# Kernel tuning notes

Hardware: AMD Instinct MI355X
Metric: run time of the kernel (lower is better)

Reference implementation:

```python
import jax, jax.numpy as jnp
import numpy as np

B, L, C, H, W = 4, 64, 64, 32, 32


def setup_inputs() -> dict:
    key = jax.random.key(0)
    ks = jax.random.split(key, 12)
    r_min, r_max = 0.8, 0.99
    u1 = jax.random.uniform(ks[0], (C, H))
    u2 = jax.random.uniform(ks[1], (C, H))
    nu_log = jnp.log(-0.5 * jnp.log(u1 * (r_max ** 2 - r_min ** 2) + r_min ** 2))
    theta_log = jnp.log(u2 * 2.0 * np.pi)
    lam_abs = jnp.exp(-jnp.exp(nu_log))  # |lambda| = exp(-exp(nu_log))
    gamma_log = jnp.log(jnp.sqrt(1.0 - lam_abs ** 2))
    params_log = jnp.concatenate([nu_log, theta_log, gamma_log], axis=0)  # (3C, H)
    s = 1.0 / np.sqrt(C)
    Wb_r = jax.random.normal(ks[2], (C, C)) * s
    Wb_i = jax.random.normal(ks[3], (C, C)) * s
    bb_r = jax.random.normal(ks[4], (C,)) * 0.01
    bb_i = jax.random.normal(ks[5], (C,)) * 0.01
    Wc_r = jax.random.normal(ks[6], (C, C)) * s
    Wc_i = jax.random.normal(ks[7], (C, C)) * s
    bc_r = jax.random.normal(ks[8], (C,)) * 0.01
    bc_i = jax.random.normal(ks[9], (C,)) * 0.01
    ln_w = jnp.ones((H, W), jnp.float32)
    ln_b = jnp.zeros((H, W), jnp.float32)
    x = jax.random.normal(ks[10], (B, L, C, H, W), jnp.float32)
    return dict(x=x, params_log=params_log, Wb_r=Wb_r, Wb_i=Wb_i, bb_r=bb_r, bb_i=bb_i,
                Wc_r=Wc_r, Wc_i=Wc_i, bc_r=bc_r, bc_i=bc_i, ln_w=ln_w, ln_b=ln_b)


def _convlru(x, params_log, Wb_r, Wb_i, bb_r, bb_i, Wc_r, Wc_i, bc_r, bc_i, ln_w, ln_b):
    c = params_log.shape[0] // 3
    p = jnp.exp(params_log)
    nu, theta, gamma = p[:c], p[c:2 * c], p[2 * c:]          # each (C, H)
    lamb = jnp.exp(-nu + 1j * theta)                          # (C, H) complex64
    # FFT over spatial dims
    h = jnp.fft.fft2(x.astype(jnp.complex64), axes=(-2, -1))  # (B,L,C,H,W)
    # proj_B: complex 1x1x1 conv == channel mixing
    Wb = Wb_r + 1j * Wb_i
    bb = bb_r + 1j * bb_i
    h = jnp.einsum('blchw,oc->blohw', h, Wb) + bb[None, None, :, None, None]
    h = h * gamma[None, None, :, :, None].astype(h.dtype)
    # parallel linear recurrence: h[t] = lamb * h[t-1] + h[t]
    a = jnp.broadcast_to(lamb[None, None, :, :, None], h.shape)

    def op(e1, e2):
        a1, b1 = e1
        a2, b2 = e2
        return (a1 * a2, a2 * b1 + b2)

    _, h = jax.lax.associative_scan(op, (a, h), axis=1)
    last_hidden_out = h[:, -1:]
    h = jnp.fft.ifft2(h, axes=(-2, -1))
    # proj_C
    Wc = Wc_r + 1j * Wc_i
    bc = bc_r + 1j * bc_i
    h = jnp.einsum('blchw,oc->blohw', h, Wc) + bc[None, None, :, None, None]
    h = h.real
    # LayerNorm over (H, W)
    mu = h.mean(axis=(-2, -1), keepdims=True)
    var = h.var(axis=(-2, -1), keepdims=True)
    h = (h - mu) * jax.lax.rsqrt(var + 1e-5) * ln_w + ln_b
    return h + x, last_hidden_out


def reference(x, params_log, Wb_r, Wb_i, bb_r, bb_i, Wc_r, Wc_i, bc_r, bc_i, ln_w, ln_b):
    return _convlru(x, params_log, Wb_r, Wb_i, bb_r, bb_i, Wc_r, Wc_i, bc_r, bc_i, ln_w, ln_b)
```

## Files before the change

kernel.cpp:

```cpp
#include <hip/hip_runtime.h>


#define NELEM 16777216
#define NIMG  16384

template <bool INV>
__device__ __forceinline__ void fft32(float2 v[32]) {
#define SW(a, b) { float2 t_ = v[a]; v[a] = v[b]; v[b] = t_; }
  SW(1, 16) SW(2, 8)  SW(3, 24) SW(5, 20) SW(6, 12) SW(7, 28)
  SW(9, 18) SW(11, 26) SW(13, 22) SW(15, 30) SW(19, 25) SW(23, 29)
#undef SW
  constexpr float TC[16] = {
      1.0f, 0.9807852804032304f, 0.9238795325112867f, 0.8314696123025452f,
      0.7071067811865476f, 0.5555702330196022f, 0.3826834323650898f, 0.1950903220161283f,
      0.0f, -0.1950903220161283f, -0.3826834323650898f, -0.5555702330196022f,
      -0.7071067811865476f, -0.8314696123025452f, -0.9238795325112867f, -0.9807852804032304f};
  constexpr float TS[16] = {
      0.0f, 0.1950903220161283f, 0.3826834323650898f, 0.5555702330196022f,
      0.7071067811865476f, 0.8314696123025452f, 0.9238795325112867f, 0.9807852804032304f,
      1.0f, 0.9807852804032304f, 0.9238795325112867f, 0.8314696123025452f,
      0.7071067811865476f, 0.5555702330196022f, 0.3826834323650898f, 0.1950903220161283f};
#pragma unroll
  for (int s = 1; s <= 5; ++s) {
    const int len = 1 << s, half = len >> 1, tstep = 32 >> s;
#pragma unroll
    for (int i = 0; i < 32; i += len) {
#pragma unroll
      for (int j = 0; j < half; ++j) {
        const int k = j * tstep;
        const float wr = TC[k];
        const float wi = INV ? TS[k] : -TS[k];
        float2 b = v[i + j + half];
        float tr = wr * b.x - wi * b.y;
        float ti = wr * b.y + wi * b.x;
        float2 a = v[i + j];
        v[i + j] = make_float2(a.x + tr, a.y + ti);
        v[i + j + half] = make_float2(a.x - tr, a.y - ti);
      }
    }
  }
}

__global__ __launch_bounds__(512) void kmix_b(const float* __restrict__ x,
                                              float2* __restrict__ A,
                                              const float* __restrict__ Wr,
                                              const float* __restrict__ Wi) {
  __shared__ float2 w[4096];
  const int t = threadIdx.x;
#pragma unroll
  for (int k = 0; k < 8; ++k) {
    int n = t + k * 512;
    w[n] = make_float2(Wr[n], Wi[n]);
  }
  __syncthreads();
  const int bl = blockIdx.x >> 3;
  const int p0 = (blockIdx.x & 7) << 7;
  const int pcol = (t & 63) * 2;
  const int obase = (t >> 6) * 8;
  const int rbase = bl * 65536 + p0 + pcol;

  float2 acc[8][2];
#pragma unroll
  for (int i = 0; i < 8; ++i) {
    acc[i][0] = make_float2(0.f, 0.f);
    acc[i][1] = make_float2(0.f, 0.f);
  }
#pragma unroll 4
  for (int c = 0; c < 64; ++c) {
    const float2 xv = *(const float2*)&x[rbase + c * 1024];
#pragma unroll
    for (int i = 0; i < 8; ++i) {
      const float2 wc = w[(obase + i) * 64 + c];
      acc[i][0].x += wc.x * xv.x; acc[i][0].y += wc.y * xv.x;
      acc[i][1].x += wc.x * xv.y; acc[i][1].y += wc.y * xv.y;
    }
  }
#pragma unroll
  for (int i = 0; i < 8; ++i) {
    float4 st = make_float4(acc[i][0].x, acc[i][0].y, acc[i][1].x, acc[i][1].y);
    *(float4*)&A[rbase + (obase + i) * 1024] = st;
  }
}

__global__ __launch_bounds__(128) void kfft_fwd(float2* __restrict__ A,
                                                const float* __restrict__ pl,
                                                const float* __restrict__ bbr,
                                                const float* __restrict__ bbi) {
  __shared__ float2 tile[4 * 1056];
  const int t = threadIdx.x;
  const int imgBase = blockIdx.x * 4096;
#pragma unroll
  for (int k = 0; k < 32; ++k) {
    int n = t + k * 128;
    float2 v = A[imgBase + n];
    int img = n >> 10, rem = n & 1023;
    tile[img * 1056 + (rem >> 5) * 33 + (rem & 31)] = v;
  }
  __syncthreads();
  const int img = t >> 5, lane = t & 31;
  {
    float2 v[32];
    float2* row = &tile[img * 1056 + lane * 33];
#pragma unroll
    for (int j = 0; j < 32; ++j) v[j] = row[j];
    fft32<false>(v);
#pragma unroll
    for (int j = 0; j < 32; ++j) row[j] = v[j];
  }
  __syncthreads();
  {
    float2 v[32];
    float2* col = &tile[img * 1056 + lane];
#pragma unroll
    for (int j = 0; j < 32; ++j) v[j] = col[j * 33];
    fft32<false>(v);
#pragma unroll
    for (int j = 0; j < 32; ++j) col[j * 33] = v[j];
  }
  __syncthreads();
#pragma unroll
  for (int k = 0; k < 32; ++k) {
    int n = t + k * 128;
    int img2 = n >> 10, rem = n & 1023, r = rem >> 5, cc = rem & 31;
    int gimg = blockIdx.x * 4 + img2;
    int ch = gimg & 63;
    float2 v = tile[img2 * 1056 + r * 33 + cc];
    float g = expf(pl[(128 + ch) * 32 + r]);
    v.x = (v.x + bbr[ch]) * g;
    v.y = (v.y + bbi[ch]) * g;
    A[imgBase + n] = v;
  }
}

template <int MODE>
__global__ __launch_bounds__(256) void kscan(float2* __restrict__ A,
                                             const float* __restrict__ pl,
                                             float* __restrict__ out1) {
  const int gid = blockIdx.x * 256 + threadIdx.x;
  const int chw = gid & 65535;
  const int b = gid >> 16;
  const int c = chw >> 10, hh = (chw >> 5) & 31;
  const float nu = expf(pl[c * 32 + hh]);
  const float th = expf(pl[2048 + c * 32 + hh]);
  const float rad = expf(-nu);
  const float lr = rad * cosf(th);
  const float li = rad * sinf(th);
  const int base = b * 4194304 + chw;
  float2 h = A[base];
#pragma unroll 4
  for (int l = 1; l < 64; ++l) {
    float2 v = A[base + l * 65536];
    float hx = lr * h.x - li * h.y + v.x;
    float hy = lr * h.y + li * h.x + v.y;
    h = make_float2(hx, hy);
    A[base + l * 65536] = h;
  }
  if (MODE == 0) {
    out1[gid] = h.x;
  } else {
    ((float2*)out1)[gid] = h;
  }
}

__global__ __launch_bounds__(512) void kmix_c(float2* __restrict__ A,
                                              const float* __restrict__ Wr,
                                              const float* __restrict__ Wi) {
  __shared__ float2 w[4096];
  const int t = threadIdx.x;
#pragma unroll
  for (int k = 0; k < 8; ++k) {
    int n = t + k * 512;
    w[n] = make_float2(Wr[n], Wi[n]);
  }
  __syncthreads();
  const int bl = blockIdx.x >> 3;
  const int p0 = (blockIdx.x & 7) << 7;
  const int pcol = (t & 63) * 2;
  const int obase = (t >> 6) * 8;
  const int rbase = bl * 65536 + p0 + pcol;

  float2 acc[8][2];
#pragma unroll
  for (int i = 0; i < 8; ++i) {
    acc[i][0] = make_float2(0.f, 0.f);
    acc[i][1] = make_float2(0.f, 0.f);
  }
#pragma unroll 4
  for (int c = 0; c < 64; ++c) {
    const float4 xv = *(const float4*)&A[rbase + c * 1024];
#pragma unroll
    for (int i = 0; i < 8; ++i) {
      const float2 wc = w[(obase + i) * 64 + c];
      acc[i][0].x += wc.x * xv.x - wc.y * xv.y;
      acc[i][0].y += wc.x * xv.y + wc.y * xv.x;
      acc[i][1].x += wc.x * xv.z - wc.y * xv.w;
      acc[i][1].y += wc.x * xv.w + wc.y * xv.z;
    }
  }
  __syncthreads();
#pragma unroll
  for (int i = 0; i < 8; ++i) {
    float4 st = make_float4(acc[i][0].x, acc[i][0].y, acc[i][1].x, acc[i][1].y);
    *(float4*)&A[rbase + (obase + i) * 1024] = st;
  }
}

__global__ __launch_bounds__(128) void kfft_inv_ln(const float2* __restrict__ A,
                                                   const float* __restrict__ x,
                                                   const float* __restrict__ bcr,
                                                   const float* __restrict__ lnw,
                                                   const float* __restrict__ lnb,
                                                   float* __restrict__ out0) {
  __shared__ float2 tile[4 * 1056];
  const int t = threadIdx.x;
  const int imgBase = blockIdx.x * 4096;
#pragma unroll
  for (int k = 0; k < 32; ++k) {
    int n = t + k * 128;
    float2 v = A[imgBase + n];
    int img = n >> 10, rem = n & 1023;
    tile[img * 1056 + (rem >> 5) * 33 + (rem & 31)] = v;
  }
  __syncthreads();
  const int img = t >> 5, lane = t & 31;
  {
    float2 v[32];
    float2* row = &tile[img * 1056 + lane * 33];
#pragma unroll
    for (int j = 0; j < 32; ++j) v[j] = row[j];
    fft32<true>(v);
#pragma unroll
    for (int j = 0; j < 32; ++j) row[j] = v[j];
  }
  __syncthreads();
  float2 v[32];
  {
    float2* col = &tile[img * 1056 + lane];
#pragma unroll
    for (int j = 0; j < 32; ++j) v[j] = col[j * 33];
    fft32<true>(v);
  }
  const int gimg = blockIdx.x * 4 + img;
  const int ch = gimg & 63;
  const float bc = bcr[ch];
  float rr[32];
  float s1 = 0.f, s2 = 0.f;
#pragma unroll
  for (int r = 0; r < 32; ++r) {
    rr[r] = v[r].x * (1.0f / 1024.0f) + bc;
    s1 += rr[r];
    s2 += rr[r] * rr[r];
  }
#pragma unroll
  for (int m = 1; m < 32; m <<= 1) {
    s1 += __shfl_xor(s1, m, 64);
    s2 += __shfl_xor(s2, m, 64);
  }
  const float mu = s1 * (1.0f / 1024.0f);
  const float var = s2 * (1.0f / 1024.0f) - mu * mu;
  const float rs = rsqrtf(var + 1e-5f);
  const int obase = gimg * 1024;
#pragma unroll
  for (int r = 0; r < 32; ++r) {
    int sp = r * 32 + lane;
    out0[obase + sp] = (rr[r] - mu) * rs * lnw[sp] + lnb[sp] + x[obase + sp];
  }
}

extern "C" void kernel_launch(void* const* d_in, const int* in_sizes, int n_in,
                              void* d_out, int out_size, void* d_ws, size_t ws_size,
                              hipStream_t stream) {
  const float* x   = (const float*)d_in[0];
  const float* pl  = (const float*)d_in[1];
  const float* Wbr = (const float*)d_in[2];
  const float* Wbi = (const float*)d_in[3];
  const float* bbr = (const float*)d_in[4];
  const float* bbi = (const float*)d_in[5];
  const float* Wcr = (const float*)d_in[6];
  const float* Wci = (const float*)d_in[7];
  const float* bcr = (const float*)d_in[8];
  const float* lnw = (const float*)d_in[10];
  const float* lnb = (const float*)d_in[11];

  float* out0 = (float*)d_out;
  float* out1 = (float*)d_out + NELEM;
  float2* A = (float2*)d_ws;

  const int tail = out_size - NELEM;

  kmix_b<<<2048, 512, 0, stream>>>(x, A, Wbr, Wbi);
  kfft_fwd<<<4096, 128, 0, stream>>>(A, pl, bbr, bbi);
  if (tail == 262144) {
    kscan<0><<<1024, 256, 0, stream>>>(A, pl, out1);
  } else {
    kscan<1><<<1024, 256, 0, stream>>>(A, pl, out1);
  }
  kmix_c<<<2048, 512, 0, stream>>>(A, Wcr, Wci);
  kfft_inv_ln<<<4096, 128, 0, stream>>>(A, x, bcr, lnw, lnb, out0);
}
```

Measured before the change: 561.1 us.

## Reorder inverse FFT before proj_C to mix real outputs only, split LayerNorm

Moves the inverse FFT ahead of the proj_C channel mix, which is valid because the mix is linear. The mix then needs only the real part of each output, computed as Wr*re - Wi*im with the 1/1024 scale folded into the weights, and it writes floats directly into the output buffer. LayerNorm becomes a separate kernel that reads that buffer back, and kmix_b is retiled to 1024 threads with 4 pixels by 4 outputs per thread. This halves the proj_C arithmetic and its output writes, at the cost of an extra full pass for LayerNorm and an extra write-back pass in the inverse FFT.

```diff
diff --git a/kernel.cpp b/kernel.cpp
--- a/kernel.cpp
+++ b/kernel.cpp
@@ -2,7 +2,6 @@
 
 
 #define NELEM 16777216
-#define NIMG  16384
 
 template <bool INV>
 __device__ __forceinline__ void fft32(float2 v[32]) {
@@ -41,44 +40,48 @@
   }
 }
 
-__global__ __launch_bounds__(512) void kmix_b(const float* __restrict__ x,
-                                              float2* __restrict__ A,
-                                              const float* __restrict__ Wr,
-                                              const float* __restrict__ Wi) {
+__global__ __launch_bounds__(1024) void kmix_b(const float* __restrict__ x,
+                                               float2* __restrict__ A,
+                                               const float* __restrict__ Wr,
+                                               const float* __restrict__ Wi) {
   __shared__ float2 w[4096];
   const int t = threadIdx.x;
 #pragma unroll
-  for (int k = 0; k < 8; ++k) {
-    int n = t + k * 512;
+  for (int k = 0; k < 4; ++k) {
+    int n = t + k * 1024;
     w[n] = make_float2(Wr[n], Wi[n]);
   }
   __syncthreads();
-  const int bl = blockIdx.x >> 3;
-  const int p0 = (blockIdx.x & 7) << 7;
-  const int pcol = (t & 63) * 2;
-  const int obase = (t >> 6) * 8;
+  const int bl = blockIdx.x >> 2;
+  const int p0 = (blockIdx.x & 3) << 8;
+  const int pcol = (t & 63) * 4;
+  const int obase = (t >> 6) * 4;
   const int rbase = bl * 65536 + p0 + pcol;
 
-  float2 acc[8][2];
-#pragma unroll
-  for (int i = 0; i < 8; ++i) {
-    acc[i][0] = make_float2(0.f, 0.f);
-    acc[i][1] = make_float2(0.f, 0.f);
-  }
+  float2 acc[4][4];
+#pragma unroll
+  for (int i = 0; i < 4; ++i)
+#pragma unroll
+    for (int p = 0; p < 4; ++p) acc[i][p] = make_float2(0.f, 0.f);
+
 #pragma unroll 4
   for (int c = 0; c < 64; ++c) {
-    const float2 xv = *(const float2*)&x[rbase + c * 1024];
-#pragma unroll
-    for (int i = 0; i < 8; ++i) {
+    const float4 xv = *(const float4*)&x[rbase + c * 1024];
+    const float xs0 = xv.x, xs1 = xv.y, xs2 = xv.z, xs3 = xv.w;
+#pragma unroll
+    for (int i = 0; i < 4; ++i) {
       const float2 wc = w[(obase + i) * 64 + c];
-      acc[i][0].x += wc.x * xv.x; acc[i][0].y += wc.y * xv.x;
-      acc[i][1].x += wc.x * xv.y; acc[i][1].y += wc.y * xv.y;
+      acc[i][0].x = fmaf(wc.x, xs0, acc[i][0].x); acc[i][0].y = fmaf(wc.y, xs0, acc[i][0].y);
+      acc[i][1].x = fmaf(wc.x, xs1, acc[i][1].x); acc[i][1].y = fmaf(wc.y, xs1, acc[i][1].y);
+      acc[i][2].x = fmaf(wc.x, xs2, acc[i][2].x); acc[i][2].y = fmaf(wc.y, xs2, acc[i][2].y);
+      acc[i][3].x = fmaf(wc.x, xs3, acc[i][3].x); acc[i][3].y = fmaf(wc.y, xs3, acc[i][3].y);
     }
   }
 #pragma unroll
-  for (int i = 0; i < 8; ++i) {
-    float4 st = make_float4(acc[i][0].x, acc[i][0].y, acc[i][1].x, acc[i][1].y);
-    *(float4*)&A[rbase + (obase + i) * 1024] = st;
+  for (int i = 0; i < 4; ++i) {
+    const int wb = rbase + (obase + i) * 1024;
+    *(float4*)&A[wb]     = make_float4(acc[i][0].x, acc[i][0].y, acc[i][1].x, acc[i][1].y);
+    *(float4*)&A[wb + 2] = make_float4(acc[i][2].x, acc[i][2].y, acc[i][3].x, acc[i][3].y);
   }
 }
 
@@ -162,55 +165,7 @@
   }
 }
 
-__global__ __launch_bounds__(512) void kmix_c(float2* __restrict__ A,
-                                              const float* __restrict__ Wr,
-                                              const float* __restrict__ Wi) {
-  __shared__ float2 w[4096];
-  const int t = threadIdx.x;
-#pragma unroll
-  for (int k = 0; k < 8; ++k) {
-    int n = t + k * 512;
-    w[n] = make_float2(Wr[n], Wi[n]);
-  }
-  __syncthreads();
-  const int bl = blockIdx.x >> 3;
-  const int p0 = (blockIdx.x & 7) << 7;
-  const int pcol = (t & 63) * 2;
-  const int obase = (t >> 6) * 8;
-  const int rbase = bl * 65536 + p0 + pcol;
-
-  float2 acc[8][2];
-#pragma unroll
-  for (int i = 0; i < 8; ++i) {
-    acc[i][0] = make_float2(0.f, 0.f);
-    acc[i][1] = make_float2(0.f, 0.f);
-  }
-#pragma unroll 4
-  for (int c = 0; c < 64; ++c) {
-    const float4 xv = *(const float4*)&A[rbase + c * 1024];
-#pragma unroll
-    for (int i = 0; i < 8; ++i) {
-      const float2 wc = w[(obase + i) * 64 + c];
-      acc[i][0].x += wc.x * xv.x - wc.y * xv.y;
-      acc[i][0].y += wc.x * xv.y + wc.y * xv.x;
-      acc[i][1].x += wc.x * xv.z - wc.y * xv.w;
-      acc[i][1].y += wc.x * xv.w + wc.y * xv.z;
-    }
-  }
-  __syncthreads();
-#pragma unroll
-  for (int i = 0; i < 8; ++i) {
-    float4 st = make_float4(acc[i][0].x, acc[i][0].y, acc[i][1].x, acc[i][1].y);
-    *(float4*)&A[rbase + (obase + i) * 1024] = st;
-  }
-}
-
-__global__ __launch_bounds__(128) void kfft_inv_ln(const float2* __restrict__ A,
-                                                   const float* __restrict__ x,
-                                                   const float* __restrict__ bcr,
-                                                   const float* __restrict__ lnw,
-                                                   const float* __restrict__ lnb,
-                                                   float* __restrict__ out0) {
+__global__ __launch_bounds__(128) void kfft_inv(float2* __restrict__ A) {
   __shared__ float2 tile[4 * 1056];
   const int t = threadIdx.x;
   const int imgBase = blockIdx.x * 4096;
@@ -233,38 +188,104 @@
     for (int j = 0; j < 32; ++j) row[j] = v[j];
   }
   __syncthreads();
-  float2 v[32];
   {
+    float2 v[32];
     float2* col = &tile[img * 1056 + lane];
 #pragma unroll
     for (int j = 0; j < 32; ++j) v[j] = col[j * 33];
     fft32<true>(v);
-  }
-  const int gimg = blockIdx.x * 4 + img;
-  const int ch = gimg & 63;
-  const float bc = bcr[ch];
-  float rr[32];
-  float s1 = 0.f, s2 = 0.f;
-#pragma unroll
-  for (int r = 0; r < 32; ++r) {
-    rr[r] = v[r].x * (1.0f / 1024.0f) + bc;
-    s1 += rr[r];
-    s2 += rr[r] * rr[r];
-  }
-#pragma unroll
-  for (int m = 1; m < 32; m <<= 1) {
+#pragma unroll
+    for (int j = 0; j < 32; ++j) col[j * 33] = v[j];
+  }
+  __syncthreads();
+#pragma unroll
+  for (int k = 0; k < 32; ++k) {
+    int n = t + k * 128;
+    int img2 = n >> 10, rem = n & 1023;
+    A[imgBase + n] = tile[img2 * 1056 + (rem >> 5) * 33 + (rem & 31)];
+  }
+}
+
+__global__ __launch_bounds__(512) void kmix_cr(const float2* __restrict__ A,
+                                               float* __restrict__ out0,
+                                               const float* __restrict__ Wr,
+                                               const float* __restrict__ Wi,
+                                               const float* __restrict__ bcr) {
+  __shared__ float2 w[4096];
+  const int t = threadIdx.x;
+  constexpr float S = 1.0f / 1024.0f;
+#pragma unroll
+  for (int k = 0; k < 8; ++k) {
+    int n = t + k * 512;
+    w[n] = make_float2(Wr[n] * S, -Wi[n] * S);
+  }
+  __syncthreads();
+  const int bl = blockIdx.x >> 2;
+  const int p0 = (blockIdx.x & 3) << 8;
+  const int pcol = (t & 63) * 4;
+  const int obase = (t >> 6) * 8;
+  const int rbase = bl * 65536 + p0 + pcol;
+
+  float acc[8][4];
+#pragma unroll
+  for (int i = 0; i < 8; ++i) {
+    const float b = bcr[obase + i];
+#pragma unroll
+    for (int p = 0; p < 4; ++p) acc[i][p] = b;
+  }
+#pragma unroll 4
+  for (int c = 0; c < 64; ++c) {
+    const float4 a0 = *(const float4*)&A[rbase + c * 1024];
+    const float4 a1 = *(const float4*)&A[rbase + c * 1024 + 2];
+#pragma unroll
+    for (int i = 0; i < 8; ++i) {
+      const float2 wc = w[(obase + i) * 64 + c];
+      acc[i][0] = fmaf(wc.x, a0.x, acc[i][0]); acc[i][0] = fmaf(wc.y, a0.y, acc[i][0]);
+      acc[i][1] = fmaf(wc.x, a0.z, acc[i][1]); acc[i][1] = fmaf(wc.y, a0.w, acc[i][1]);
+      acc[i][2] = fmaf(wc.x, a1.x, acc[i][2]); acc[i][2] = fmaf(wc.y, a1.y, acc[i][2]);
+      acc[i][3] = fmaf(wc.x, a1.z, acc[i][3]); acc[i][3] = fmaf(wc.y, a1.w, acc[i][3]);
+    }
+  }
+  const int wb = bl * 65536 + p0 + pcol;
+#pragma unroll
+  for (int i = 0; i < 8; ++i) {
+    *(float4*)&out0[wb + (obase + i) * 1024] =
+        make_float4(acc[i][0], acc[i][1], acc[i][2], acc[i][3]);
+  }
+}
+
+__global__ __launch_bounds__(256) void k_ln(float* __restrict__ out0,
+                                            const float* __restrict__ x,
+                                            const float* __restrict__ lnw,
+                                            const float* __restrict__ lnb) {
+  __shared__ float red[8];
+  const int t = threadIdx.x;
+  const int base = blockIdx.x * 1024;
+  const int sp = t * 4;
+  float4 v = *(const float4*)&out0[base + sp];
+  float s1 = v.x + v.y + v.z + v.w;
+  float s2 = v.x * v.x + v.y * v.y + v.z * v.z + v.w * v.w;
+#pragma unroll
+  for (int m = 1; m < 64; m <<= 1) {
     s1 += __shfl_xor(s1, m, 64);
     s2 += __shfl_xor(s2, m, 64);
   }
+  if ((t & 63) == 0) { red[(t >> 6) * 2] = s1; red[(t >> 6) * 2 + 1] = s2; }
+  __syncthreads();
+  s1 = red[0] + red[2] + red[4] + red[6];
+  s2 = red[1] + red[3] + red[5] + red[7];
   const float mu = s1 * (1.0f / 1024.0f);
   const float var = s2 * (1.0f / 1024.0f) - mu * mu;
   const float rs = rsqrtf(var + 1e-5f);
-  const int obase = gimg * 1024;
-#pragma unroll
-  for (int r = 0; r < 32; ++r) {
-    int sp = r * 32 + lane;
-    out0[obase + sp] = (rr[r] - mu) * rs * lnw[sp] + lnb[sp] + x[obase + sp];
-  }
+  const float4 xv = *(const float4*)&x[base + sp];
+  const float4 lw = *(const float4*)&lnw[sp];
+  const float4 lb = *(const float4*)&lnb[sp];
+  float4 o;
+  o.x = (v.x - mu) * rs * lw.x + lb.x + xv.x;
+  o.y = (v.y - mu) * rs * lw.y + lb.y + xv.y;
+  o.z = (v.z - mu) * rs * lw.z + lb.z + xv.z;
+  o.w = (v.w - mu) * rs * lw.w + lb.w + xv.w;
+  *(float4*)&out0[base + sp] = o;
 }
 
 extern "C" void kernel_launch(void* const* d_in, const int* in_sizes, int n_in,
@@ -288,13 +309,14 @@
 
   const int tail = out_size - NELEM;
 
-  kmix_b<<<2048, 512, 0, stream>>>(x, A, Wbr, Wbi);
+  kmix_b<<<1024, 1024, 0, stream>>>(x, A, Wbr, Wbi);
   kfft_fwd<<<4096, 128, 0, stream>>>(A, pl, bbr, bbi);
   if (tail == 262144) {
     kscan<0><<<1024, 256, 0, stream>>>(A, pl, out1);
   } else {
     kscan<1><<<1024, 256, 0, stream>>>(A, pl, out1);
   }
-  kmix_c<<<2048, 512, 0, stream>>>(A, Wcr, Wci);
-  kfft_inv_ln<<<4096, 128, 0, stream>>>(A, x, bcr, lnw, lnb, out0);
-}
+  kfft_inv<<<4096, 128, 0, stream>>>(A);
+  kmix_cr<<<1024, 512, 0, stream>>>(A, out0, Wcr, Wci, bcr);
+  k_ln<<<16384, 256, 0, stream>>>(out0, x, lnw, lnb);
+}
```

New measurement: 479.2 us. -14.6%, faster.
